# Kernel tuning notes

Measured on AMD Instinct MI355X. Metric: run time of the kernel, lower is better.

## Reference

```python
import jax, jax.numpy as jnp
import numpy as np

N, B, L, C, H = 16384, 16, 32, 256, 8
DH = C // H
K_STATIC = 16   # k_max for L=32 (L>20 -> min(16, L//2))
K_MIN = 8       # int(0.25*L)
LN_EPS = 1e-5


def _ln(x, g, b):
    m = x.mean(-1, keepdims=True)
    v = ((x - m) ** 2).mean(-1, keepdims=True)
    return (x - m) / jnp.sqrt(v + LN_EPS) * g + b


def setup_inputs() -> dict:
    key = jax.random.key(0)
    ks = jax.random.split(key, 12)
    s = 1.0 / np.sqrt(C)
    f32 = jnp.float32
    return {
        'vision_features': jax.random.normal(ks[0], (N, B, C), dtype=f32),
        'text_features': jax.random.normal(ks[1], (L, B, C), dtype=f32),
        'vp_w': jax.random.normal(ks[2], (C, C), dtype=f32) * s,
        'vp_b': jnp.zeros((C,), f32),
        'tp_w': jax.random.normal(ks[3], (C, C), dtype=f32) * s,
        'tp_b': jnp.zeros((C,), f32),
        'in_proj_w': jax.random.normal(ks[4], (3 * C, C), dtype=f32) * s,
        'in_proj_b': jnp.zeros((3 * C,), f32),
        'w1': jax.random.normal(ks[5], (C, C), dtype=f32) * s,
        'b1': jnp.zeros((C,), f32),
        'g1': jnp.ones((C,), f32),
        'be1': jnp.zeros((C,), f32),
        'w2': jax.random.normal(ks[6], (C // 2, C), dtype=f32) * s,
        'b2': jnp.zeros((C // 2,), f32),
        'g2': jnp.ones((C // 2,), f32),
        'be2': jnp.zeros((C // 2,), f32),
        'w3': jax.random.normal(ks[7], (1, C // 2), dtype=f32) * s,
        'b3': jnp.zeros((1,), f32),
        'k_weight': jnp.asarray(np.log(0.4 / 0.6), f32),
        'alpha_coarse': jnp.asarray(np.log(0.72 / 0.28), f32),
        'alpha_fine': jnp.asarray(np.log(0.82 / 0.18), f32),
    }


def reference(vision_features, text_features, vp_w, vp_b, tp_w, tp_b,
              in_proj_w, in_proj_b, w1, b1, g1, be1, w2, b2, g2, be2,
              w3, b3, k_weight, alpha_coarse, alpha_fine):
    # projections (torch Linear: y = x W^T + b)
    vision_proj = vision_features @ vp_w.T + vp_b  # [N,B,C]
    text_proj = text_features @ tp_w.T + tp_b      # [L,B,C]

    # nn.MultiheadAttention attention weights, averaged over heads
    qp = vision_proj @ in_proj_w[:C].T + in_proj_b[:C]
    kp = text_proj @ in_proj_w[C:2 * C].T + in_proj_b[C:2 * C]
    q = qp.reshape(N, B, H, DH)
    k = kp.reshape(L, B, H, DH)
    scores = jnp.einsum('nbhd,lbhd->bhnl', q, k) / np.sqrt(DH)
    attn = jax.nn.softmax(scores, axis=-1).mean(axis=1)  # [B,N,L]

    # data-dependent k_top per batch (unbiased variance over L, mean over N)
    mu = attn.mean(axis=-1, keepdims=True)
    var = ((attn - mu) ** 2).sum(axis=-1) / (L - 1)       # [B,N]
    attn_variance = var.mean(axis=1)                      # [B]
    k_ws = jax.nn.sigmoid(k_weight)
    ratio = jnp.clip(k_ws * (1.0 + attn_variance * 0.5), 0.25, 0.6)
    k_base = jnp.maximum(1, jnp.floor(L * ratio).astype(jnp.int32))
    k_top = jnp.maximum(K_MIN, jnp.minimum(jnp.minimum(K_STATIC, k_base), L))  # [B]

    # variable-k top-k via static K_STATIC + mask
    top = -jnp.sort(-attn, axis=-1)[..., :K_STATIC]       # [B,N,K]
    mask = jnp.arange(K_STATIC)[None, None, :] < k_top[:, None, None]
    logits = jnp.where(mask, top, -jnp.inf)
    w = jax.nn.softmax(logits, axis=-1)
    similarity_score = jnp.sum(jnp.where(mask, top * w, 0.0), axis=-1)  # [B,N]

    # importance MLP on raw vision features (dropout off at inference)
    h = jax.nn.relu(_ln(vision_features @ w1.T + b1, g1, be1))
    h = jax.nn.relu(_ln(h @ w2.T + b2, g2, be2))
    feature_importance = jax.nn.sigmoid(h @ w3.T + b3)[..., 0]  # [N,B]
    feature_importance = feature_importance.T                    # [B,N]

    def minmax(x):
        lo = x.min(axis=1, keepdims=True)
        rng = x.max(axis=1, keepdims=True) - lo
        return jnp.where(rng > 0, (x - lo) / rng, 0.0)

    sim_norm = minmax(similarity_score)
    imp_norm = minmax(feature_importance)

    alpha = (jax.nn.sigmoid(alpha_coarse) + jax.nn.sigmoid(alpha_fine)) / 2.0
    importance = alpha * sim_norm + (1.0 - alpha) * imp_norm  # [B,N]
    return importance.T  # [N,B]
```

## Files before the change

### kernel.cpp

```cpp
#include <hip/hip_runtime.h>
#include <hip/hip_bf16.h>

typedef _Float16 f16;
typedef _Float16 half8 __attribute__((ext_vector_type(8)));
typedef _Float16 half4 __attribute__((ext_vector_type(4)));
typedef float f32x4 __attribute__((ext_vector_type(4)));

typedef const __attribute__((address_space(1))) void gvoid;
typedef __attribute__((address_space(3))) void lvoid;
#define GLOAD16(src, dst) __builtin_amdgcn_global_load_lds((gvoid*)(src), (lvoid*)(dst), 16, 0, 0)

#define WQV_OFF   0u
#define WKT_OFF   262144u
#define KP_OFF    524288u
#define W2S_OFF   1048576u
#define SBIAS_OFF 3145728u
#define BQV_OFF   3162112u
#define BKT_OFF   3163136u
#define W1H_OFF   3164160u
#define W2H_OFF   3295232u
#define VARP_OFF  3360768u
#define SMM_OFF   3377280u
#define FMM_OFF   3377408u
#define CAND_OFF  3377664u
#define FI_OFF    12814848u
#define SIM_OFF   13863424u

__device__ __forceinline__ float sigm(float x) { return 1.f / (1.f + __expf(-x)); }
__device__ __forceinline__ unsigned fmap(float f) {
  unsigned u = __float_as_uint(f);
  return (u & 0x80000000u) ? ~u : (u | 0x80000000u);
}
__device__ __forceinline__ float funmap(unsigned u) {
  unsigned b = (u & 0x80000000u) ? (u & 0x7FFFFFFFu) : ~u;
  return __uint_as_float(b);
}

__global__ void k_p1(const float* __restrict__ ipw, const float* __restrict__ ipb,
                     const float* __restrict__ vp_w, const float* __restrict__ vp_b,
                     const float* __restrict__ tp_w, const float* __restrict__ tp_b,
                     float* __restrict__ Wqv, float* __restrict__ Wkt,
                     float* __restrict__ bqv, float* __restrict__ bkt,
                     unsigned* __restrict__ simMM, unsigned* __restrict__ fiMM) {
  int tx = threadIdx.x, ty = threadIdx.y;
  int bz = blockIdx.z;
  if (bz == 2) {
    if (blockIdx.x || blockIdx.y) return;
    if (ty == 0 && tx < 16) {
      simMM[tx * 2] = 0xFFFFFFFFu; simMM[tx * 2 + 1] = 0u;
      fiMM[tx * 2] = 0xFFFFFFFFu;  fiMM[tx * 2 + 1] = 0u;
    }
    int j = ty * 16 + tx;
    float s1 = 0.f, s2 = 0.f;
    for (int k = 0; k < 256; ++k) {
      s1 += ipw[j * 256 + k] * vp_b[k];
      s2 += ipw[65536 + j * 256 + k] * tp_b[k];
    }
    bqv[j] = s1 + ipb[j];
    bkt[j] = s2 + ipb[256 + j];
    return;
  }
  const float* A = ipw + (bz ? 65536 : 0);
  const float* B = bz ? tp_w : vp_w;
  float* O = bz ? Wkt : Wqv;
  __shared__ float As[16][16], Bs[16][17];
  int row = blockIdx.y * 16 + ty, col = blockIdx.x * 16 + tx;
  float s = 0.f;
  for (int tt = 0; tt < 16; ++tt) {
    As[ty][tx] = A[row * 256 + tt * 16 + tx];
    Bs[ty][tx] = B[(tt * 16 + ty) * 256 + col];
    __syncthreads();
#pragma unroll
    for (int k = 0; k < 16; ++k) s += As[ty][k] * Bs[k][tx];
    __syncthreads();
  }
  O[row * 256 + col] = s;
}

__global__ void k_conv(const float* __restrict__ w1, const float* __restrict__ w2,
                       char* __restrict__ W1g, char* __restrict__ W2g) {
  int i = blockIdx.x * 256 + threadIdx.x;
  if (i < 65536) {
    int o = i >> 8, c = i & 255;
    *(f16*)(W1g + (c >> 6) * 32768 + o * 128 + (((c & 63) << 1) ^ ((o & 7) << 4))) = (f16)w1[i];
  } else if (i < 98304) {
    int i2 = i - 65536;
    int o = i2 >> 8, c = i2 & 255;
    *(f16*)(W2g + (c >> 6) * 16384 + o * 128 + (((c & 63) << 1) ^ ((o & 7) << 4))) = (f16)w2[i2];
  }
}

__global__ void k_p2(const float* __restrict__ T, const float* __restrict__ Wkt,
                     const float* __restrict__ bkt, float* __restrict__ kp) {
  __shared__ float As[16][16], Ws[16][17];
  int tx = threadIdx.x, ty = threadIdx.y;
  int lb = blockIdx.y * 16 + ty;
  int i = blockIdx.x * 16 + tx;
  float s = 0.f;
  for (int tt = 0; tt < 16; ++tt) {
    As[ty][tx] = T[(size_t)lb * 256 + tt * 16 + tx];
    Ws[ty][tx] = Wkt[(size_t)(blockIdx.x * 16 + ty) * 256 + tt * 16 + tx];
    __syncthreads();
#pragma unroll
    for (int k = 0; k < 16; ++k) s += As[ty][k] * Ws[tx][k];
    __syncthreads();
  }
  kp[(size_t)lb * 256 + i] = s + bkt[i];
}

__global__ void k_p3(const float* __restrict__ kp, const float* __restrict__ Wqv,
                     const float* __restrict__ bqv, char* __restrict__ W2sg,
                     float* __restrict__ sbias) {
  const float SC = 0.17677669529663687f;
  int b = blockIdx.z, jt = blockIdx.y, ct = blockIdx.x;
  int ty = threadIdx.y, tx = threadIdx.x;
  int j2 = jt * 16 + ty, c = ct * 16 + tx;
  int h = j2 >> 5, l = j2 & 31;
  const float* kr = kp + (size_t)(l * 16 + b) * 256 + h * 32;
  const float* wq = Wqv + (size_t)h * 32 * 256 + c;
  float s = 0.f;
#pragma unroll
  for (int d = 0; d < 32; ++d) s += kr[d] * wq[(size_t)d * 256];
  *(f16*)(W2sg + (size_t)b * 131072 + (c >> 6) * 32768 + j2 * 128 +
          (((c & 63) << 1) ^ ((j2 & 7) << 4))) = (f16)(s * SC);
  if (ct == 0 && tx == 0) {
    float sb = 0.f;
#pragma unroll
    for (int d = 0; d < 32; ++d) sb += kr[d] * bqv[h * 32 + d];
    sbias[b * 256 + j2] = sb * SC;
  }
}

__global__ void __launch_bounds__(256, 3) k_main(
    const float* __restrict__ X, const char* __restrict__ W2sg,
    const float* __restrict__ sbias,
    const char* __restrict__ W1g, const char* __restrict__ W2g,
    const float* __restrict__ b1, const float* __restrict__ g1, const float* __restrict__ be1,
    const float* __restrict__ b2, const float* __restrict__ g2, const float* __restrict__ be2,
    const float* __restrict__ w3, const float* __restrict__ b3,
    float* __restrict__ cand, float* __restrict__ varpart, float* __restrict__ fi) {
  __shared__ __align__(16) char smem[49152];
  __shared__ float pSQ[2][64][5];
  __shared__ float pM[64], pR[64];
  const int b = blockIdx.y;
  const int bx = blockIdx.x;
  const int n0 = bx * 64;
  const int t = threadIdx.x;
  const int w = t >> 6;
  const int lane = t & 63;
  const int ln = lane & 15, kg = lane >> 4;
  char* AT = smem;
  char* BT = smem + 8192;

  auto issueA = [&](int kt) {
    int row = t >> 2, cq = t & 3;
    const float* Xr = X + ((size_t)(n0 + row) * 16 + b) * 256 + kt * 64 + cq * 16;
    f32x4 a0 = *(const f32x4*)(Xr), a1 = *(const f32x4*)(Xr + 4);
    f32x4 a2 = *(const f32x4*)(Xr + 8), a3 = *(const f32x4*)(Xr + 12);
    half8 h0, h1;
#pragma unroll
    for (int i = 0; i < 4; ++i) {
      h0[i] = (f16)a0[i]; h0[4 + i] = (f16)a1[i];
      h1[i] = (f16)a2[i]; h1[4 + i] = (f16)a3[i];
    }
    unsigned sw = (unsigned)((row & 7) << 4);
    *(half8*)(AT + ((unsigned)(row * 128 + cq * 32) ^ sw)) = h0;
    *(half8*)(AT + ((unsigned)(row * 128 + cq * 32 + 16) ^ sw)) = h1;
  };

  if (blockIdx.z == 0) {
    const char* Wb = W2sg + (size_t)b * 131072;
    auto issueB = [&](int kt) {
      const char* src = Wb + kt * 32768 + w * 8192 + (lane << 4);
      char* dst = BT + w * 8192;
#pragma unroll
      for (int i = 0; i < 8; ++i) GLOAD16(src + i * 1024, dst + i * 1024);
    };

    f32x4 acc[4][4];
#pragma unroll
    for (int q = 0; q < 4; ++q)
#pragma unroll
      for (int ni = 0; ni < 4; ++ni)
#pragma unroll
        for (int i = 0; i < 4; ++i) acc[q][ni][i] = 0.f;

    issueA(0); issueB(0);
    __syncthreads();
#pragma unroll
    for (int kt = 0; kt < 4; ++kt) {
      half8 av[4][2], bv[4][2];
#pragma unroll
      for (int q = 0; q < 4; ++q) {
        int o = w * 64 + q * 16 + ln;
        unsigned sw = (unsigned)((o & 7) << 4);
#pragma unroll
        for (int mi = 0; mi < 2; ++mi)
          av[q][mi] = *(const half8*)(BT + o * 128 + ((unsigned)(mi * 64 + kg * 16) ^ sw));
      }
#pragma unroll
      for (int ni = 0; ni < 4; ++ni) {
        int n = ni * 16 + ln;
        unsigned sw = (unsigned)((n & 7) << 4);
#pragma unroll
        for (int mi = 0; mi < 2; ++mi)
          bv[ni][mi] = *(const half8*)(AT + n * 128 + ((unsigned)(mi * 64 + kg * 16) ^ sw));
      }
#pragma unroll
      for (int mi = 0; mi < 2; ++mi)
#pragma unroll
        for (int q = 0; q < 4; ++q)
#pragma unroll
          for (int ni = 0; ni < 4; ++ni)
            acc[q][ni] = __builtin_amdgcn_mfma_f32_16x16x32_f16(av[q][mi], bv[ni][mi], acc[q][ni], 0, 0, 0);
      __syncthreads();
      if (kt < 3) { issueA(kt + 1); issueB(kt + 1); __syncthreads(); }
    }

    {
      f32x4 sb[4];
#pragma unroll
      for (int q = 0; q < 4; ++q)
        sb[q] = *(const f32x4*)(sbias + b * 256 + (w * 4 + q) * 16 + kg * 4);
      float vm[4][2][4];
#pragma unroll
      for (int ni = 0; ni < 4; ++ni)
#pragma unroll
        for (int qq = 0; qq < 2; ++qq)
#pragma unroll
          for (int r = 0; r < 4; ++r) vm[ni][qq][r] = 0.f;
#pragma unroll
      for (int hh = 0; hh < 2; ++hh)
#pragma unroll
        for (int ni = 0; ni < 4; ++ni) {
          float x[2][4];
          float mx = -1e30f;
#pragma unroll
          for (int qq = 0; qq < 2; ++qq)
#pragma unroll
            for (int r = 0; r < 4; ++r) {
              x[qq][r] = acc[hh * 2 + qq][ni][r] + sb[hh * 2 + qq][r];
              mx = fmaxf(mx, x[qq][r]);
            }
          mx = fmaxf(mx, __shfl_xor(mx, 16, 64));
          mx = fmaxf(mx, __shfl_xor(mx, 32, 64));
          float S = 0.f;
#pragma unroll
          for (int qq = 0; qq < 2; ++qq)
#pragma unroll
            for (int r = 0; r < 4; ++r) { x[qq][r] = __expf(x[qq][r] - mx); S += x[qq][r]; }
          S += __shfl_xor(S, 16, 64);
          S += __shfl_xor(S, 32, 64);
          float inv = 0.125f / S;
#pragma unroll
          for (int qq = 0; qq < 2; ++qq)
#pragma unroll
            for (int r = 0; r < 4; ++r) vm[ni][qq][r] += x[qq][r] * inv;
        }
      float* slice = (float*)(smem + 8192) + w * 2048;
#pragma unroll
      for (int ni = 0; ni < 4; ++ni)
#pragma unroll
        for (int qq = 0; qq < 2; ++qq)
#pragma unroll
          for (int r = 0; r < 4; ++r)
            slice[(qq * 16 + kg * 4 + r) * 64 + ni * 16 + ln] = vm[ni][qq][r];
    }
    __syncthreads();

    if (w == 0) {
      const float* sl = (const float*)(smem + 8192);
      float v[32];
#pragma unroll
      for (int l = 0; l < 32; ++l)
        v[l] = sl[l * 64 + lane] + sl[2048 + l * 64 + lane] +
               sl[4096 + l * 64 + lane] + sl[6144 + l * 64 + lane];
      float s2 = 0.f;
#pragma unroll
      for (int l = 0; l < 32; ++l) s2 += v[l] * v[l];
      float vr = (s2 - (1.f / 32.f)) * (1.f / 31.f);
#pragma unroll
      for (int m = 1; m < 64; m <<= 1) vr += __shfl_xor(vr, m, 64);
      if (lane == 0) varpart[b * 256 + bx] = vr;
#pragma unroll
      for (int k = 2; k <= 32; k <<= 1) {
#pragma unroll
        for (int j = k >> 1; j > 0; j >>= 1) {
#pragma unroll
          for (int i = 0; i < 32; ++i) {
            int l = i ^ j;
            if (l > i) {
              float a = v[i], c = v[l];
              float hi = fmaxf(a, c), lo = fminf(a, c);
              bool up = ((i & k) == 0);
              v[i] = up ? hi : lo;
              v[l] = up ? lo : hi;
            }
          }
        }
      }
      float m0 = v[0], se = 0.f, te = 0.f;
      float cn[9];
#pragma unroll
      for (int i = 0; i < 16; ++i) {
        float e = __expf(v[i] - m0);
        se += e; te += v[i] * e;
        if (i >= 7) cn[i - 7] = te / se;
      }
#pragma unroll
      for (int i = 0; i < 9; ++i)
        cand[(size_t)i * 262144 + (size_t)b * 16384 + n0 + lane] = cn[i];
    }
    return;
  }

  char* H1 = smem;
  char* W2T = smem + 32768;
  auto issueB1 = [&](int kt) {
    const char* src = W1g + kt * 32768 + w * 8192 + (lane << 4);
    char* dst = BT + w * 8192;
#pragma unroll
    for (int i = 0; i < 8; ++i) GLOAD16(src + i * 1024, dst + i * 1024);
  };
  auto issueW2 = [&](int kt) {
    const char* src = W2g + kt * 16384 + w * 4096 + (lane << 4);
    char* dst = W2T + w * 4096;
    GLOAD16(src, dst);
    GLOAD16(src + 1024, dst + 1024);
    GLOAD16(src + 2048, dst + 2048);
    GLOAD16(src + 3072, dst + 3072);
  };

  f32x4 acc[4][4];
#pragma unroll
  for (int q = 0; q < 4; ++q)
#pragma unroll
    for (int ni = 0; ni < 4; ++ni)
#pragma unroll
      for (int i = 0; i < 4; ++i) acc[q][ni][i] = 0.f;

  issueA(0); issueB1(0);
  __syncthreads();
#pragma unroll
  for (int kt = 0; kt < 4; ++kt) {
    half8 av[4][2], bv[4][2];
#pragma unroll
    for (int q = 0; q < 4; ++q) {
      int o = w * 64 + q * 16 + ln;
      unsigned sw = (unsigned)((o & 7) << 4);
#pragma unroll
      for (int mi = 0; mi < 2; ++mi)
        av[q][mi] = *(const half8*)(BT + o * 128 + ((unsigned)(mi * 64 + kg * 16) ^ sw));
    }
#pragma unroll
    for (int ni = 0; ni < 4; ++ni) {
      int n = ni * 16 + ln;
      unsigned sw = (unsigned)((n & 7) << 4);
#pragma unroll
      for (int mi = 0; mi < 2; ++mi)
        bv[ni][mi] = *(const half8*)(AT + n * 128 + ((unsigned)(mi * 64 + kg * 16) ^ sw));
    }
#pragma unroll
    for (int mi = 0; mi < 2; ++mi)
#pragma unroll
      for (int q = 0; q < 4; ++q)
#pragma unroll
        for (int ni = 0; ni < 4; ++ni)
          acc[q][ni] = __builtin_amdgcn_mfma_f32_16x16x32_f16(av[q][mi], bv[ni][mi], acc[q][ni], 0, 0, 0);
    __syncthreads();
    if (kt < 3) { issueA(kt + 1); issueB1(kt + 1); __syncthreads(); }
  }
  issueW2(0);

  {
    f32x4 b1v[4];
#pragma unroll
    for (int q = 0; q < 4; ++q)
      b1v[q] = *(const f32x4*)(b1 + (w * 4 + q) * 16 + kg * 4);
#pragma unroll
    for (int ni = 0; ni < 4; ++ni) {
      float s = 0.f, qq = 0.f;
#pragma unroll
      for (int q = 0; q < 4; ++q)
#pragma unroll
        for (int r = 0; r < 4; ++r) {
          float v = acc[q][ni][r] + b1v[q][r];
          acc[q][ni][r] = v;
          s += v; qq += v * v;
        }
      s += __shfl_xor(s, 16, 64); s += __shfl_xor(s, 32, 64);
      qq += __shfl_xor(qq, 16, 64); qq += __shfl_xor(qq, 32, 64);
      if (kg == 0) { int n = ni * 16 + ln; pSQ[0][n][w] = s; pSQ[1][n][w] = qq; }
    }
  }
  __syncthreads();
  if (t < 64) {
    float s = pSQ[0][t][0] + pSQ[0][t][1] + pSQ[0][t][2] + pSQ[0][t][3];
    float q = pSQ[1][t][0] + pSQ[1][t][1] + pSQ[1][t][2] + pSQ[1][t][3];
    float mean = s * (1.f / 256.f);
    float var = q * (1.f / 256.f) - mean * mean;
    pM[t] = mean;
    pR[t] = rsqrtf(var + 1e-5f);
  }
  __syncthreads();

  {
    f32x4 g1v[4], e1v[4];
#pragma unroll
    for (int q = 0; q < 4; ++q) {
      g1v[q] = *(const f32x4*)(g1 + (w * 4 + q) * 16 + kg * 4);
      e1v[q] = *(const f32x4*)(be1 + (w * 4 + q) * 16 + kg * 4);
    }
#pragma unroll
    for (int ni = 0; ni < 4; ++ni) {
      int n = ni * 16 + ln;
      float mean = pM[n], rstd = pR[n];
      unsigned sw = (unsigned)((n & 7) << 4);
#pragma unroll
      for (int q = 0; q < 4; ++q) {
        half4 hv;
#pragma unroll
        for (int r = 0; r < 4; ++r) {
          float y = (acc[q][ni][r] - mean) * rstd * g1v[q][r] + e1v[q][r];
          hv[r] = (f16)fmaxf(y, 0.f);
        }
        *(half4*)(H1 + ((unsigned)(n * 512 + (w * 4 + q) * 32 + kg * 8) ^ sw)) = hv;
      }
    }
  }
  __syncthreads();

  f32x4 acc2[2][4];
#pragma unroll
  for (int oi = 0; oi < 2; ++oi)
#pragma unroll
    for (int ni = 0; ni < 4; ++ni)
#pragma unroll
      for (int i = 0; i < 4; ++i) acc2[oi][ni][i] = 0.f;
#pragma unroll
  for (int kt = 0; kt < 4; ++kt) {
    half8 a2[2][2], bv[4][2];
#pragma unroll
    for (int oi = 0; oi < 2; ++oi) {
      int o2 = w * 32 + oi * 16 + ln;
      unsigned sw = (unsigned)((o2 & 7) << 4);
#pragma unroll
      for (int mi = 0; mi < 2; ++mi)
        a2[oi][mi] = *(const half8*)(W2T + o2 * 128 + ((unsigned)(mi * 64 + kg * 16) ^ sw));
    }
#pragma unroll
    for (int ni = 0; ni < 4; ++ni) {
      int n = ni * 16 + ln;
      unsigned sw = (unsigned)((n & 7) << 4);
#pragma unroll
      for (int mi = 0; mi < 2; ++mi)
        bv[ni][mi] = *(const half8*)(H1 + n * 512 + kt * 128 + ((unsigned)(mi * 64 + kg * 16) ^ sw));
    }
#pragma unroll
    for (int mi = 0; mi < 2; ++mi)
#pragma unroll
      for (int oi = 0; oi < 2; ++oi)
#pragma unroll
        for (int ni = 0; ni < 4; ++ni)
          acc2[oi][ni] = __builtin_amdgcn_mfma_f32_16x16x32_f16(a2[oi][mi], bv[ni][mi], acc2[oi][ni], 0, 0, 0);
    __syncthreads();
    if (kt < 3) { issueW2(kt + 1); __syncthreads(); }
  }

  {
    f32x4 b2v[2], g2v[2], e2v[2], w3v[2];
#pragma unroll
    for (int oi = 0; oi < 2; ++oi) {
      b2v[oi] = *(const f32x4*)(b2 + (w * 2 + oi) * 16 + kg * 4);
      g2v[oi] = *(const f32x4*)(g2 + (w * 2 + oi) * 16 + kg * 4);
      e2v[oi] = *(const f32x4*)(be2 + (w * 2 + oi) * 16 + kg * 4);
      w3v[oi] = *(const f32x4*)(w3 + (w * 2 + oi) * 16 + kg * 4);
    }
#pragma unroll
    for (int ni = 0; ni < 4; ++ni) {
      float s = 0.f, q = 0.f;
#pragma unroll
      for (int oi = 0; oi < 2; ++oi)
#pragma unroll
        for (int r = 0; r < 4; ++r) {
          float v = acc2[oi][ni][r] + b2v[oi][r];
          acc2[oi][ni][r] = v;
          s += v; q += v * v;
        }
      s += __shfl_xor(s, 16, 64); s += __shfl_xor(s, 32, 64);
      q += __shfl_xor(q, 16, 64); q += __shfl_xor(q, 32, 64);
      if (kg == 0) { int n = ni * 16 + ln; pSQ[0][n][w] = s; pSQ[1][n][w] = q; }
    }
    __syncthreads();
    if (t < 64) {
      float s = pSQ[0][t][0] + pSQ[0][t][1] + pSQ[0][t][2] + pSQ[0][t][3];
      float q = pSQ[1][t][0] + pSQ[1][t][1] + pSQ[1][t][2] + pSQ[1][t][3];
      float mean = s * (1.f / 128.f);
      float var = q * (1.f / 128.f) - mean * mean;
      pM[t] = mean;
      pR[t] = rsqrtf(var + 1e-5f);
    }
    __syncthreads();
#pragma unroll
    for (int ni = 0; ni < 4; ++ni) {
      int n = ni * 16 + ln;
      float mean = pM[n], rstd = pR[n];
      float a3 = 0.f;
#pragma unroll
      for (int oi = 0; oi < 2; ++oi)
#pragma unroll
        for (int r = 0; r < 4; ++r) {
          float y = (acc2[oi][ni][r] - mean) * rstd * g2v[oi][r] + e2v[oi][r];
          a3 += fmaxf(y, 0.f) * w3v[oi][r];
        }
      a3 += __shfl_xor(a3, 16, 64);
      a3 += __shfl_xor(a3, 32, 64);
      if (kg == 0) pSQ[0][n][w] = a3;
    }
    __syncthreads();
    if (t < 64) {
      float z = pSQ[0][t][0] + pSQ[0][t][1] + pSQ[0][t][2] + pSQ[0][t][3] + b3[0];
      fi[(size_t)b * 16384 + n0 + t] = sigm(z);
    }
  }
}

__global__ void __launch_bounds__(256) k_g4(
    const float* __restrict__ cand, const float* __restrict__ fi,
    const float* __restrict__ varpart, const float* __restrict__ kw,
    float* __restrict__ sim, unsigned* __restrict__ simMM, unsigned* __restrict__ fiMM) {
  __shared__ float red[4][4];
  __shared__ int kS;
  int b = blockIdx.x >> 6;
  if (threadIdx.x < 64) {
    float s = 0.f;
#pragma unroll
    for (int i = 0; i < 4; ++i) s += varpart[b * 256 + threadIdx.x + i * 64];
#pragma unroll
    for (int m = 1; m < 64; m <<= 1) s += __shfl_xor(s, m, 64);
    if (threadIdx.x == 0) {
      float var = s * (1.f / 16384.f);
      float kws = sigm(kw[0]);
      float ratio = fminf(fmaxf(kws * (1.f + var * 0.5f), 0.25f), 0.6f);
      int kb = (int)floorf(32.f * ratio);
      if (kb < 1) kb = 1;
      int kt = kb < 16 ? kb : 16;
      if (kt < 8) kt = 8;
      kS = kt;
    }
  }
  __syncthreads();
  int k = kS;
  int n = (blockIdx.x & 63) * 256 + threadIdx.x;
  size_t idx = (size_t)b * 16384 + n;
  float sv = cand[(size_t)(k - 8) * 262144 + idx];
  sim[idx] = sv;
  float fv = fi[idx];
  float sn = sv, sx = sv, fn = fv, fx = fv;
#pragma unroll
  for (int m = 1; m < 64; m <<= 1) {
    sn = fminf(sn, __shfl_xor(sn, m, 64));
    sx = fmaxf(sx, __shfl_xor(sx, m, 64));
    fn = fminf(fn, __shfl_xor(fn, m, 64));
    fx = fmaxf(fx, __shfl_xor(fx, m, 64));
  }
  int wv = threadIdx.x >> 6;
  if ((threadIdx.x & 63) == 0) { red[0][wv] = sn; red[1][wv] = sx; red[2][wv] = fn; red[3][wv] = fx; }
  __syncthreads();
  if (threadIdx.x == 0) {
    float a = red[0][0], c = red[1][0], d = red[2][0], e = red[3][0];
#pragma unroll
    for (int i = 1; i < 4; ++i) {
      a = fminf(a, red[0][i]); c = fmaxf(c, red[1][i]);
      d = fminf(d, red[2][i]); e = fmaxf(e, red[3][i]);
    }
    atomicMin(&simMM[b * 2 + 0], fmap(a));
    atomicMax(&simMM[b * 2 + 1], fmap(c));
    atomicMin(&fiMM[b * 2 + 0], fmap(d));
    atomicMax(&fiMM[b * 2 + 1], fmap(e));
  }
}

__global__ void __launch_bounds__(256) k_g5(
    const float* __restrict__ sim, const float* __restrict__ fi,
    const unsigned* __restrict__ simMM, const unsigned* __restrict__ fiMM,
    const float* __restrict__ ac, const float* __restrict__ af,
    float* __restrict__ out) {
  __shared__ float ls[256][17], lf[256][17];
  __shared__ float sMin[16], sInv[16], fMin[16], fInv[16];
  int t = threadIdx.x;
  int n0 = blockIdx.x * 256;
  if (t < 16) {
    float lo = funmap(simMM[t * 2]), hi = funmap(simMM[t * 2 + 1]);
    float r = hi - lo;
    sMin[t] = lo; sInv[t] = (r > 0.f) ? 1.f / r : 0.f;
    lo = funmap(fiMM[t * 2]); hi = funmap(fiMM[t * 2 + 1]);
    r = hi - lo;
    fMin[t] = lo; fInv[t] = (r > 0.f) ? 1.f / r : 0.f;
  }
#pragma unroll
  for (int i = 0; i < 16; ++i) {
    ls[t][i] = sim[(size_t)i * 16384 + n0 + t];
    lf[t][i] = fi[(size_t)i * 16384 + n0 + t];
  }
  __syncthreads();
  float alpha = 0.5f * (sigm(ac[0]) + sigm(af[0]));
  float o[16];
#pragma unroll
  for (int b = 0; b < 16; ++b) {
    float s = (ls[t][b] - sMin[b]) * sInv[b];
    float f = (lf[t][b] - fMin[b]) * fInv[b];
    o[b] = alpha * s + (1.f - alpha) * f;
  }
  float* op = out + (size_t)(n0 + t) * 16;
#pragma unroll
  for (int i = 0; i < 4; ++i) {
    f32x4 v;
    v[0] = o[i * 4]; v[1] = o[i * 4 + 1]; v[2] = o[i * 4 + 2]; v[3] = o[i * 4 + 3];
    *(f32x4*)(op + i * 4) = v;
  }
}

extern "C" void kernel_launch(void* const* d_in, const int* in_sizes, int n_in,
                              void* d_out, int out_size, void* d_ws, size_t ws_size,
                              hipStream_t stream) {
  const float* X    = (const float*)d_in[0];
  const float* T    = (const float*)d_in[1];
  const float* vp_w = (const float*)d_in[2];
  const float* vp_b = (const float*)d_in[3];
  const float* tp_w = (const float*)d_in[4];
  const float* tp_b = (const float*)d_in[5];
  const float* ipw  = (const float*)d_in[6];
  const float* ipb  = (const float*)d_in[7];
  const float* w1   = (const float*)d_in[8];
  const float* b1   = (const float*)d_in[9];
  const float* g1   = (const float*)d_in[10];
  const float* be1  = (const float*)d_in[11];
  const float* w2   = (const float*)d_in[12];
  const float* b2   = (const float*)d_in[13];
  const float* g2   = (const float*)d_in[14];
  const float* be2  = (const float*)d_in[15];
  const float* w3   = (const float*)d_in[16];
  const float* b3   = (const float*)d_in[17];
  const float* kw   = (const float*)d_in[18];
  const float* ac   = (const float*)d_in[19];
  const float* af   = (const float*)d_in[20];
  char* ws = (char*)d_ws;
  float* Wqv = (float*)(ws + WQV_OFF);
  float* Wkt = (float*)(ws + WKT_OFF);
  float* kp = (float*)(ws + KP_OFF);
  char* W2sg = ws + W2S_OFF;
  float* sbias = (float*)(ws + SBIAS_OFF);
  float* bqv = (float*)(ws + BQV_OFF);
  float* bkt = (float*)(ws + BKT_OFF);
  char* W1g = ws + W1H_OFF;
  char* W2g = ws + W2H_OFF;
  float* varpart = (float*)(ws + VARP_OFF);
  unsigned* simMM = (unsigned*)(ws + SMM_OFF);
  unsigned* fiMM = (unsigned*)(ws + FMM_OFF);
  float* cand = (float*)(ws + CAND_OFF);
  float* fi = (float*)(ws + FI_OFF);
  float* sim = (float*)(ws + SIM_OFF);
  float* out = (float*)d_out;

  k_p1<<<dim3(16, 16, 3), dim3(16, 16), 0, stream>>>(ipw, ipb, vp_w, vp_b, tp_w, tp_b,
                                                     Wqv, Wkt, bqv, bkt, simMM, fiMM);
  k_conv<<<384, 256, 0, stream>>>(w1, w2, W1g, W2g);
  k_p2<<<dim3(16, 32), dim3(16, 16), 0, stream>>>(T, Wkt, bkt, kp);
  k_p3<<<dim3(16, 16, 16), dim3(16, 16), 0, stream>>>(kp, Wqv, bqv, W2sg, sbias);
  k_main<<<dim3(256, 16, 2), 256, 0, stream>>>(X, W2sg, sbias, W1g, W2g,
                                               b1, g1, be1, b2, g2, be2, w3, b3,
                                               cand, varpart, fi);
  k_g4<<<1024, 256, 0, stream>>>(cand, fi, varpart, kw, sim, simMM, fiMM);
  k_g5<<<64, 256, 0, stream>>>(sim, fi, simMM, fiMM, ac, af, out);
}
```

Before: 250.0 us.

## Load W2 MFMA fragments directly from global and shrink LDS for occupancy

Repacks W2 into a fragment-ordered layout so each lane reads its MFMA A-operand straight from global memory (a 1KB contiguous block per fragment) instead of staging W2 tiles through LDS. This removes the W2 LDS buffer and its per-k-step barriers. The LN scratch arrays are folded into the freed shared region, which cuts the static LDS from about 49KB to 40KB, and launch bounds are raised to 4 blocks per SM. The trade-off is that W2 global reads now sit directly in the MFMA loop, relying on L2/L1 hits, and the tighter register budget may cause spills.

```diff
diff --git a/kernel.cpp b/kernel.cpp
--- a/kernel.cpp
+++ b/kernel.cpp
@@ -35,6 +35,11 @@
   unsigned b = (u & 0x80000000u) ? (u & 0x7FFFFFFFu) : ~u;
   return __uint_as_float(b);
 }
+__device__ __forceinline__ unsigned fragoff(int o, int c) {
+  int ot = o >> 4, ln = o & 15;
+  int kc = c >> 6, mi = (c >> 5) & 1, kg = (c >> 3) & 3, h8 = c & 7;
+  return (unsigned)((((ot * 4 + kc) * 2 + mi) << 10) + ((kg * 16 + ln) << 4) + h8 * 2);
+}
 
 __global__ void k_p1(const float* __restrict__ ipw, const float* __restrict__ ipb,
                      const float* __restrict__ vp_w, const float* __restrict__ vp_b,
@@ -86,7 +91,7 @@
   } else if (i < 98304) {
     int i2 = i - 65536;
     int o = i2 >> 8, c = i2 & 255;
-    *(f16*)(W2g + (c >> 6) * 16384 + o * 128 + (((c & 63) << 1) ^ ((o & 7) << 4))) = (f16)w2[i2];
+    *(f16*)(W2g + fragoff(o, c)) = (f16)w2[i2];
   }
 }
 
@@ -131,7 +136,7 @@
   }
 }
 
-__global__ void __launch_bounds__(256, 3) k_main(
+__global__ void __launch_bounds__(256, 4) k_main(
     const float* __restrict__ X, const char* __restrict__ W2sg,
     const float* __restrict__ sbias,
     const char* __restrict__ W1g, const char* __restrict__ W2g,
@@ -139,9 +144,7 @@
     const float* __restrict__ b2, const float* __restrict__ g2, const float* __restrict__ be2,
     const float* __restrict__ w3, const float* __restrict__ b3,
     float* __restrict__ cand, float* __restrict__ varpart, float* __restrict__ fi) {
-  __shared__ __align__(16) char smem[49152];
-  __shared__ float pSQ[2][64][5];
-  __shared__ float pM[64], pR[64];
+  __shared__ __align__(16) char smem[40960];
   const int b = blockIdx.y;
   const int bx = blockIdx.x;
   const int n0 = bx * 64;
@@ -315,21 +318,16 @@
   }
 
   char* H1 = smem;
-  char* W2T = smem + 32768;
+  float* pS = (float*)(smem + 32768);
+  float* pQ = (float*)(smem + 34048);
+  float* pM = (float*)(smem + 35328);
+  float* pR = (float*)(smem + 35584);
   auto issueB1 = [&](int kt) {
     const char* src = W1g + kt * 32768 + w * 8192 + (lane << 4);
     char* dst = BT + w * 8192;
 #pragma unroll
     for (int i = 0; i < 8; ++i) GLOAD16(src + i * 1024, dst + i * 1024);
   };
-  auto issueW2 = [&](int kt) {
-    const char* src = W2g + kt * 16384 + w * 4096 + (lane << 4);
-    char* dst = W2T + w * 4096;
-    GLOAD16(src, dst);
-    GLOAD16(src + 1024, dst + 1024);
-    GLOAD16(src + 2048, dst + 2048);
-    GLOAD16(src + 3072, dst + 3072);
-  };
 
   f32x4 acc[4][4];
 #pragma unroll
@@ -370,7 +368,6 @@
     __syncthreads();
     if (kt < 3) { issueA(kt + 1); issueB1(kt + 1); __syncthreads(); }
   }
-  issueW2(0);
 
   {
     f32x4 b1v[4];
@@ -390,13 +387,13 @@
         }
       s += __shfl_xor(s, 16, 64); s += __shfl_xor(s, 32, 64);
       qq += __shfl_xor(qq, 16, 64); qq += __shfl_xor(qq, 32, 64);
-      if (kg == 0) { int n = ni * 16 + ln; pSQ[0][n][w] = s; pSQ[1][n][w] = qq; }
+      if (kg == 0) { int n = ni * 16 + ln; pS[n * 5 + w] = s; pQ[n * 5 + w] = qq; }
     }
   }
   __syncthreads();
   if (t < 64) {
-    float s = pSQ[0][t][0] + pSQ[0][t][1] + pSQ[0][t][2] + pSQ[0][t][3];
-    float q = pSQ[1][t][0] + pSQ[1][t][1] + pSQ[1][t][2] + pSQ[1][t][3];
+    float s = pS[t * 5 + 0] + pS[t * 5 + 1] + pS[t * 5 + 2] + pS[t * 5 + 3];
+    float q = pQ[t * 5 + 0] + pQ[t * 5 + 1] + pQ[t * 5 + 2] + pQ[t * 5 + 3];
     float mean = s * (1.f / 256.f);
     float var = q * (1.f / 256.f) - mean * mean;
     pM[t] = mean;
@@ -441,13 +438,10 @@
   for (int kt = 0; kt < 4; ++kt) {
     half8 a2[2][2], bv[4][2];
 #pragma unroll
-    for (int oi = 0; oi < 2; ++oi) {
-      int o2 = w * 32 + oi * 16 + ln;
-      unsigned sw = (unsigned)((o2 & 7) << 4);
+    for (int oi = 0; oi < 2; ++oi)
 #pragma unroll
       for (int mi = 0; mi < 2; ++mi)
-        a2[oi][mi] = *(const half8*)(W2T + o2 * 128 + ((unsigned)(mi * 64 + kg * 16) ^ sw));
-    }
+        a2[oi][mi] = *(const half8*)(W2g + ((((w * 2 + oi) * 4 + kt) * 2 + mi) << 10) + (lane << 4));
 #pragma unroll
     for (int ni = 0; ni < 4; ++ni) {
       int n = ni * 16 + ln;
@@ -463,8 +457,6 @@
 #pragma unroll
         for (int ni = 0; ni < 4; ++ni)
           acc2[oi][ni] = __builtin_amdgcn_mfma_f32_16x16x32_f16(a2[oi][mi], bv[ni][mi], acc2[oi][ni], 0, 0, 0);
-    __syncthreads();
-    if (kt < 3) { issueW2(kt + 1); __syncthreads(); }
   }
 
   {
@@ -476,6 +468,7 @@
       e2v[oi] = *(const f32x4*)(be2 + (w * 2 + oi) * 16 + kg * 4);
       w3v[oi] = *(const f32x4*)(w3 + (w * 2 + oi) * 16 + kg * 4);
     }
+    __syncthreads();
 #pragma unroll
     for (int ni = 0; ni < 4; ++ni) {
       float s = 0.f, q = 0.f;
@@ -489,12 +482,12 @@
         }
       s += __shfl_xor(s, 16, 64); s += __shfl_xor(s, 32, 64);
       q += __shfl_xor(q, 16, 64); q += __shfl_xor(q, 32, 64);
-      if (kg == 0) { int n = ni * 16 + ln; pSQ[0][n][w] = s; pSQ[1][n][w] = q; }
+      if (kg == 0) { int n = ni * 16 + ln; pS[n * 5 + w] = s; pQ[n * 5 + w] = q; }
     }
     __syncthreads();
     if (t < 64) {
-      float s = pSQ[0][t][0] + pSQ[0][t][1] + pSQ[0][t][2] + pSQ[0][t][3];
-      float q = pSQ[1][t][0] + pSQ[1][t][1] + pSQ[1][t][2] + pSQ[1][t][3];
+      float s = pS[t * 5 + 0] + pS[t * 5 + 1] + pS[t * 5 + 2] + pS[t * 5 + 3];
+      float q = pQ[t * 5 + 0] + pQ[t * 5 + 1] + pQ[t * 5 + 2] + pQ[t * 5 + 3];
       float mean = s * (1.f / 128.f);
       float var = q * (1.f / 128.f) - mean * mean;
       pM[t] = mean;
@@ -515,11 +508,11 @@
         }
       a3 += __shfl_xor(a3, 16, 64);
       a3 += __shfl_xor(a3, 32, 64);
-      if (kg == 0) pSQ[0][n][w] = a3;
+      if (kg == 0) pS[n * 5 + w] = a3;
     }
     __syncthreads();
     if (t < 64) {
-      float z = pSQ[0][t][0] + pSQ[0][t][1] + pSQ[0][t][2] + pSQ[0][t][3] + b3[0];
+      float z = pS[t * 5 + 0] + pS[t * 5 + 1] + pS[t * 5 + 2] + pS[t * 5 + 3] + b3[0];
       fi[(size_t)b * 16384 + n0 + t] = sigm(z);
     }
   }
```

After: 257.4 us. 3.0% more time.
